# Kernel optimization log

Hardware: AMD Instinct MI355X
Metric: run time of the kernel (lower is better)

## Reference

```python
import jax, jax.numpy as jnp
import numpy as np

MAX_LEN = 3

def _attention(h, enc, w1, b1, w2):
    # h: [B,H], enc: [B,S,H]
    B, S, H = enc.shape
    hs = jnp.broadcast_to(h[:, None, :], (B, S, H))
    x = jnp.tanh(jnp.concatenate([enc, hs], axis=-1) @ w1.T + b1)  # [B,S,H]
    e = (x @ w2.T)[..., 0]                                         # [B,S]
    alpha = jax.nn.softmax(e, axis=1)
    return jnp.einsum('bs,bsd->bd', alpha, enc)                    # [B,H]

def _gru_cell(x, h, w_ih, w_hh, b_ih, b_hh):
    # torch GRU gate order: r, z, n
    H = h.shape[-1]
    gi = x @ w_ih.T + b_ih   # [B,3H]
    gh = h @ w_hh.T + b_hh
    i_r, i_z, i_n = gi[:, :H], gi[:, H:2*H], gi[:, 2*H:]
    h_r, h_z, h_n = gh[:, :H], gh[:, H:2*H], gh[:, 2*H:]
    r = jax.nn.sigmoid(i_r + h_r)
    z = jax.nn.sigmoid(i_z + h_z)
    n = jnp.tanh(i_n + r * h_n)
    return (1.0 - z) * n + z * h

def setup_inputs() -> dict:
    key = jax.random.key(0)
    ks = jax.random.split(key, 16)
    B, S, H, DW = 1024, 40, 1024, 512
    V0 = V1 = 4000
    EMB_N = V0 + V1 + 1
    sc = lambda fan: 1.0 / np.sqrt(fan)
    inp = {
        'encoder_outputs': jax.random.normal(ks[0], (B, S, H), jnp.float32),
        'encoder_hidden': jax.random.normal(ks[1], (1, B, H), jnp.float32),
        'targets': jax.random.randint(ks[2], (MAX_LEN, B), 0, V0),
        'emb': jax.random.normal(ks[3], (EMB_N, DW), jnp.float32) * 0.02,
        'attn_w1': jax.random.normal(ks[4], (H, 2 * H), jnp.float32) * sc(2 * H),
        'attn_b1': jnp.zeros((H,), jnp.float32),
        'attn_w2': jax.random.normal(ks[5], (1, H), jnp.float32) * sc(H),
        'w_ih': jax.random.normal(ks[6], (3 * H, H + DW), jnp.float32) * sc(H),
        'w_hh': jax.random.normal(ks[7], (3 * H, H), jnp.float32) * sc(H),
        'b_ih': jnp.zeros((3 * H,), jnp.float32),
        'b_hh': jnp.zeros((3 * H,), jnp.float32),
        'out0_w': jax.random.normal(ks[8], (V0, H), jnp.float32) * sc(H),
        'out0_b': jnp.zeros((V0,), jnp.float32),
        'out1_w': jax.random.normal(ks[9], (V1, H), jnp.float32) * sc(H),
        'out1_b': jnp.zeros((V1,), jnp.float32),
    }
    return inp

def reference(encoder_outputs, encoder_hidden, targets, emb, attn_w1, attn_b1,
              attn_w2, w_ih, w_hh, b_ih, b_hh, out0_w, out0_b, out1_w, out1_b):
    B = encoder_outputs.shape[0]
    h = encoder_hidden[0]  # n_layers=1, unidirectional -> init state passthrough
    logs = []
    for t in range(MAX_LEN):
        context = _attention(h, encoder_outputs, attn_w1, attn_b1, attn_w2)
        if t == 0:
            it = jnp.zeros((B,), jnp.int32)
        elif t == 1:
            it = targets[0] + 1
        else:
            it = targets[t - 1] + 36
        x = jnp.concatenate([emb[it], context], axis=1)  # [B, DW+H]
        h = _gru_cell(x, h, w_ih, w_hh, b_ih, b_hh)
        if t == 0 or t == 2:
            logits = h @ out0_w.T + out0_b
        else:
            logits = h @ out1_w.T + out1_b
        logs.append(jax.nn.log_softmax(logits, axis=1))
    return jnp.stack(logs)  # [MAX_LEN, B, V]
```

## Files before the change

kernel.cpp:

```cpp
#include <hip/hip_runtime.h>
#include <hip/hip_bf16.h>
#include <math.h>

#define B_SZ 1024
#define S_SZ 40
#define H_SZ 1024
#define DW_SZ 512
#define V_SZ 4000
#define XW (DW_SZ + H_SZ)
#define NGL 8192

typedef __bf16 bf16x8 __attribute__((ext_vector_type(8)));
typedef float f32x4 __attribute__((ext_vector_type(4)));

__device__ __forceinline__ float fast_tanh(float x) {
    return 1.0f - 2.0f / (1.0f + __expf(2.0f * x));
}
__device__ __forceinline__ float fast_sigmoid(float x) {
    return 1.0f / (1.0f + __expf(-x));
}
__device__ __forceinline__ float bfraw2f(unsigned short u) {
    return __uint_as_float(((unsigned)u) << 16);
}
__device__ __forceinline__ ushort4 cvt4(float4 v) {
    union { ushort4 u; __hip_bfloat16 h[4]; } o;
    o.h[0] = __float2bfloat16(v.x); o.h[1] = __float2bfloat16(v.y);
    o.h[2] = __float2bfloat16(v.z); o.h[3] = __float2bfloat16(v.w);
    return o.u;
}

#define GLL16(gp, lp)                                                                \
    __builtin_amdgcn_global_load_lds((const __attribute__((address_space(1))) void*)(gp), \
                                     (__attribute__((address_space(3))) void*)(lp), 16, 0, 0)

__global__ __launch_bounds__(256, 2) void gemm_bt_pipe128(
    const __hip_bfloat16* __restrict__ A, int lda,
    const __hip_bfloat16* __restrict__ W, int ldw,
    const float* __restrict__ bias,
    __hip_bfloat16* __restrict__ C, int ldc,
    int nbx, int K) {
    extern __shared__ char smem[];
    const int tid = threadIdx.x;
    const int lane = tid & 63;
    const int wave = tid >> 6;
    const int wm = wave >> 1, wn = wave & 1;
    const int fr = lane & 15, fq = lane >> 4;

    int bid = blockIdx.x;
    { const int cpx = gridDim.x >> 3; bid = (bid & 7) * cpx + (bid >> 3); }
    const int by = bid / nbx;
    const int bm = by * 128;
    const int bn = (bid - by * nbx) * 256;

    const int r0 = tid >> 2;
    const int s0 = (tid & 3) ^ ((tid >> 3) & 3);
    const __hip_bfloat16* gA0 = A + (size_t)(bm + r0) * lda + s0 * 8;
    const __hip_bfloat16* gA1 = A + (size_t)(bm + r0 + 64) * lda + s0 * 8;
    const __hip_bfloat16* gW0 = W + (size_t)(bn + r0) * ldw + s0 * 8;
    const __hip_bfloat16* gW1 = W + (size_t)(bn + r0 + 64) * ldw + s0 * 8;
    const __hip_bfloat16* gW2 = W + (size_t)(bn + r0 + 128) * ldw + s0 * 8;
    const __hip_bfloat16* gW3 = W + (size_t)(bn + r0 + 192) * ldw + s0 * 8;
    const int dst0 = tid * 16;

    int aoff[4], boff[8];
#pragma unroll
    for (int mi = 0; mi < 4; ++mi) {
        const int row = wm * 64 + mi * 16 + fr;
        aoff[mi] = row * 64 + ((fq ^ ((row >> 1) & 3)) << 4);
    }
#pragma unroll
    for (int ni = 0; ni < 8; ++ni) {
        const int col = wn * 128 + ni * 16 + fr;
        boff[ni] = 8192 + col * 64 + ((fq ^ ((col >> 1) & 3)) << 4);
    }

    const int NT = K >> 5;
    f32x4 acc[4][8] = {};

#define STAGE_T(t)                                                    \
    do {                                                              \
        char* sb = smem + ((t) % 3) * 24576;                          \
        const int kk = (t) << 5;                                      \
        GLL16(gA0 + kk, sb + dst0);                                   \
        GLL16(gA1 + kk, sb + dst0 + 4096);                            \
        GLL16(gW0 + kk, sb + 8192 + dst0);                            \
        GLL16(gW1 + kk, sb + 8192 + dst0 + 4096);                     \
        GLL16(gW2 + kk, sb + 8192 + dst0 + 8192);                     \
        GLL16(gW3 + kk, sb + 8192 + dst0 + 12288);                    \
    } while (0)

    STAGE_T(0);
    STAGE_T(1);
    __builtin_amdgcn_sched_barrier(0);
    asm volatile("s_waitcnt vmcnt(6)" ::: "memory");
    __builtin_amdgcn_s_barrier();
    __builtin_amdgcn_sched_barrier(0);

    for (int t = 0; t < NT; ++t) {
        const char* sb = smem + (t % 3) * 24576;
        bf16x8 af[4], bg[8];
#pragma unroll
        for (int ni = 0; ni < 8; ++ni) bg[ni] = *reinterpret_cast<const bf16x8*>(sb + boff[ni]);
#pragma unroll
        for (int mi = 0; mi < 4; ++mi) af[mi] = *reinterpret_cast<const bf16x8*>(sb + aoff[mi]);

        if (t + 2 < NT) STAGE_T(t + 2);

        __builtin_amdgcn_s_setprio(1);
#pragma unroll
        for (int mi = 0; mi < 4; ++mi)
#pragma unroll
            for (int ni = 0; ni < 8; ++ni)
                acc[mi][ni] = __builtin_amdgcn_mfma_f32_16x16x32_bf16(af[mi], bg[ni], acc[mi][ni], 0, 0, 0);
        __builtin_amdgcn_s_setprio(0);

        if (t != NT - 1) {
            __builtin_amdgcn_sched_barrier(0);
            if (t + 2 < NT) asm volatile("s_waitcnt vmcnt(6)" ::: "memory");
            else            asm volatile("s_waitcnt vmcnt(0)" ::: "memory");
            __builtin_amdgcn_s_barrier();
            __builtin_amdgcn_sched_barrier(0);
        }
    }
#undef STAGE_T

#pragma unroll
    for (int ni = 0; ni < 8; ++ni) {
        const int col = bn + wn * 128 + ni * 16 + fr;
        const float bb = bias ? bias[col] : 0.0f;
#pragma unroll
        for (int mi = 0; mi < 4; ++mi) {
            const int row0 = bm + wm * 64 + mi * 16 + fq * 4;
#pragma unroll
            for (int r = 0; r < 4; ++r)
                C[(size_t)(row0 + r) * ldc + col] = __float2bfloat16(acc[mi][ni][r] + bb);
        }
    }
}

#define SB0 0
#define SB1 10240
#define SB2 10496
#define SB3 10752
#define SB4 11520
#define SB5 12672
#define SB6 13672
#define SB7 14672
#define SB8 14696
#define SBTOT 14720
__global__ __launch_bounds__(256) void cast_fast_kernel(
    const float* __restrict__ enc, const float* __restrict__ w1,
    const float* __restrict__ whh, const float* __restrict__ wih,
    const float* __restrict__ o0, const float* __restrict__ o1,
    __hip_bfloat16* __restrict__ enc_bf, __hip_bfloat16* __restrict__ w1a_bf,
    __hip_bfloat16* __restrict__ wall0, __hip_bfloat16* __restrict__ wall1,
    __hip_bfloat16* __restrict__ wih_bf) {
    const int blk = blockIdx.x;
    const int tid = threadIdx.x;
    ushort4* w0u = reinterpret_cast<ushort4*>(wall0);
    ushort4* w1u = reinterpret_cast<ushort4*>(wall1);

    if (blk < SB1) {
        const int li = blk * 1024 + tid;
        const float4* s = reinterpret_cast<const float4*>(enc);
        float4 v0 = s[li], v1 = s[li + 256], v2 = s[li + 512], v3 = s[li + 768];
        ushort4* d = reinterpret_cast<ushort4*>(enc_bf);
        d[li] = cvt4(v0); d[li + 256] = cvt4(v1); d[li + 512] = cvt4(v2); d[li + 768] = cvt4(v3);
    } else if (blk < SB2) {
        const int r0 = (blk - SB1) * 4;
        const float4* s = reinterpret_cast<const float4*>(w1);
        float4 v0 = s[(r0 + 0) * 512 + tid], v1 = s[(r0 + 1) * 512 + tid],
               v2 = s[(r0 + 2) * 512 + tid], v3 = s[(r0 + 3) * 512 + tid];
        ushort4* d = reinterpret_cast<ushort4*>(w1a_bf);
        const int li = r0 * 256 + tid;
        d[li] = cvt4(v0); d[li + 256] = cvt4(v1); d[li + 512] = cvt4(v2); d[li + 768] = cvt4(v3);
    } else if (blk < SB3) {
        const int r0 = (blk - SB2) * 4;
        const float4* s = reinterpret_cast<const float4*>(w1);
        ushort4 u0 = cvt4(s[(r0 + 0) * 512 + 256 + tid]), u1 = cvt4(s[(r0 + 1) * 512 + 256 + tid]),
                u2 = cvt4(s[(r0 + 2) * 512 + 256 + tid]), u3 = cvt4(s[(r0 + 3) * 512 + 256 + tid]);
        const int li = r0 * 256 + tid;
        w0u[li] = u0; w0u[li + 256] = u1; w0u[li + 512] = u2; w0u[li + 768] = u3;
        w1u[li] = u0; w1u[li + 256] = u1; w1u[li + 512] = u2; w1u[li + 768] = u3;
    } else if (blk < SB4) {
        const int li = (blk - SB3) * 1024 + tid;
        const float4* s = reinterpret_cast<const float4*>(whh);
        ushort4 u0 = cvt4(s[li]), u1 = cvt4(s[li + 256]), u2 = cvt4(s[li + 512]), u3 = cvt4(s[li + 768]);
        w0u[262144 + li] = u0; w0u[262144 + li + 256] = u1;
        w0u[262144 + li + 512] = u2; w0u[262144 + li + 768] = u3;
        w1u[262144 + li] = u0; w1u[262144 + li + 256] = u1;
        w1u[262144 + li + 512] = u2; w1u[262144 + li + 768] = u3;
    } else if (blk < SB5) {
        const int li = (blk - SB4) * 1024 + tid;
        const float4* s = reinterpret_cast<const float4*>(wih);
        float4 v0 = s[li], v1 = s[li + 256], v2 = s[li + 512], v3 = s[li + 768];
        ushort4* d = reinterpret_cast<ushort4*>(wih_bf);
        d[li] = cvt4(v0); d[li + 256] = cvt4(v1); d[li + 512] = cvt4(v2); d[li + 768] = cvt4(v3);
    } else if (blk < SB6) {
        const int li = (blk - SB5) * 1024 + tid;
        const float4* s = reinterpret_cast<const float4*>(o0);
        float4 v0 = s[li], v1 = s[li + 256], v2 = s[li + 512], v3 = s[li + 768];
        w0u[1048576 + li] = cvt4(v0); w0u[1048576 + li + 256] = cvt4(v1);
        w0u[1048576 + li + 512] = cvt4(v2); w0u[1048576 + li + 768] = cvt4(v3);
    } else if (blk < SB7) {
        const int li = (blk - SB6) * 1024 + tid;
        const float4* s = reinterpret_cast<const float4*>(o1);
        float4 v0 = s[li], v1 = s[li + 256], v2 = s[li + 512], v3 = s[li + 768];
        w1u[1048576 + li] = cvt4(v0); w1u[1048576 + li + 256] = cvt4(v1);
        w1u[1048576 + li + 512] = cvt4(v2); w1u[1048576 + li + 768] = cvt4(v3);
    } else {
        const ushort4 z = make_ushort4(0, 0, 0, 0);
        if (blk < SB8) {
            const int li = 2072576 + (blk - SB7) * 1024 + tid;
            w0u[li] = z; w0u[li + 256] = z; w0u[li + 512] = z; w0u[li + 768] = z;
        } else {
            const int li = 2072576 + (blk - SB8) * 1024 + tid;
            w1u[li] = z; w1u[li + 256] = z; w1u[li + 512] = z; w1u[li + 768] = z;
        }
    }
}

__global__ __launch_bounds__(256) void small_prep_kernel(
    const float* __restrict__ emb, const int* __restrict__ targets,
    __hip_bfloat16* __restrict__ x0, __hip_bfloat16* __restrict__ x1, __hip_bfloat16* __restrict__ x2,
    const float* __restrict__ enc_h, float* __restrict__ h, __hip_bfloat16* __restrict__ h_bf,
    const float* __restrict__ b1, const float* __restrict__ b_hh,
    const float* __restrict__ o0b, const float* __restrict__ o1b,
    float* __restrict__ bias0, float* __restrict__ bias1) {
    const int blk = blockIdx.x;
    const int tid = threadIdx.x;
    if (blk < 3072) {
        if (tid >= 128) return;
        const int t = blk >> 10;
        const int b = blk & 1023;
        int it; __hip_bfloat16* x;
        if (t == 0) { it = 0; x = x0; }
        else if (t == 1) { it = targets[b] + 1; x = x1; }
        else { it = targets[B_SZ + b] + 36; x = x2; }
        float4 v = reinterpret_cast<const float4*>(emb + (size_t)it * DW_SZ)[tid];
        reinterpret_cast<ushort4*>(x + (size_t)b * XW)[tid] = cvt4(v);
    } else if (blk < 4096) {
        const int i = (blk - 3072) * 256 + tid;
        const float4 v = reinterpret_cast<const float4*>(enc_h)[i];
        reinterpret_cast<float4*>(h)[i] = v;
        reinterpret_cast<ushort4*>(h_bf)[i] = cvt4(v);
    } else {
        float* bt = (blk == 4096) ? bias0 : bias1;
        const float* ob = (blk == 4096) ? o0b : o1b;
        for (int j = tid; j < NGL; j += 256) {
            float v;
            if (j < H_SZ) v = b1[j];
            else if (j < 4 * H_SZ) v = b_hh[j - H_SZ];
            else if (j < 4 * H_SZ + V_SZ) v = ob[j - 4 * H_SZ];
            else v = 0.0f;
            bt[j] = v;
        }
    }
}

__global__ __launch_bounds__(256) void attn_ls_kernel(
    const __hip_bfloat16* __restrict__ enc,
    const __hip_bfloat16* __restrict__ enc_proj,
    const __hip_bfloat16* __restrict__ hgl,
    const float* __restrict__ w2,
    __hip_bfloat16* __restrict__ x,
    float* __restrict__ outp,
    int nattn) {
    const int blk = blockIdx.x;
    const int tid = threadIdx.x;
    const int lane = tid & 63, wave = tid >> 6;
    __shared__ float s_e[S_SZ];
    __shared__ float s_red[4];
    __shared__ float s_bc;

    if (blk < nattn) {
        const int b = blk;
        float hp[16], wv[16];
        const unsigned short* hgrow = reinterpret_cast<const unsigned short*>(hgl) + (size_t)b * NGL;
#pragma unroll
        for (int p = 0; p < 4; ++p) {
            const int base = p * 256 + lane * 4;
            ushort4 hu = *reinterpret_cast<const ushort4*>(hgrow + base);
            float4 wq = *reinterpret_cast<const float4*>(w2 + base);
            hp[p * 4 + 0] = bfraw2f(hu.x); hp[p * 4 + 1] = bfraw2f(hu.y);
            hp[p * 4 + 2] = bfraw2f(hu.z); hp[p * 4 + 3] = bfraw2f(hu.w);
            wv[p * 4 + 0] = wq.x; wv[p * 4 + 1] = wq.y;
            wv[p * 4 + 2] = wq.z; wv[p * 4 + 3] = wq.w;
        }

        const unsigned short* ep0 = reinterpret_cast<const unsigned short*>(enc_proj) + (size_t)b * S_SZ * H_SZ;
#pragma unroll 2
        for (int i = 0; i < 10; ++i) {
            const int s = wave + 4 * i;
            const unsigned short* row = ep0 + (size_t)s * H_SZ;
            float acc = 0.f;
#pragma unroll
            for (int p = 0; p < 4; ++p) {
                ushort4 eu = *reinterpret_cast<const ushort4*>(row + p * 256 + lane * 4);
                acc += fast_tanh(bfraw2f(eu.x) + hp[p * 4 + 0]) * wv[p * 4 + 0]
                     + fast_tanh(bfraw2f(eu.y) + hp[p * 4 + 1]) * wv[p * 4 + 1]
                     + fast_tanh(bfraw2f(eu.z) + hp[p * 4 + 2]) * wv[p * 4 + 2]
                     + fast_tanh(bfraw2f(eu.w) + hp[p * 4 + 3]) * wv[p * 4 + 3];
            }
#pragma unroll
            for (int off = 32; off > 0; off >>= 1) acc += __shfl_down(acc, off);
            if (lane == 0) s_e[s] = acc;
        }
        __syncthreads();

        float m = -1e30f;
        for (int s = 0; s < S_SZ; ++s) m = fmaxf(m, s_e[s]);
        float sum = 0.f;
        for (int s = 0; s < S_SZ; ++s) sum += __expf(s_e[s] - m);
        const float inv = 1.0f / sum;

        const ushort4* enc_b = reinterpret_cast<const ushort4*>(enc + (size_t)b * S_SZ * H_SZ);
        float4 acc = make_float4(0.f, 0.f, 0.f, 0.f);
        for (int s = 0; s < S_SZ; ++s) {
            const float a = __expf(s_e[s] - m) * inv;
            ushort4 ev = enc_b[s * 256 + tid];
            acc.x += a * bfraw2f(ev.x); acc.y += a * bfraw2f(ev.y);
            acc.z += a * bfraw2f(ev.z); acc.w += a * bfraw2f(ev.w);
        }
        reinterpret_cast<ushort4*>(x + (size_t)b * XW + DW_SZ)[tid] = cvt4(acc);
    } else {
        const int b = blk - nattn;
        const ushort4* row4 = reinterpret_cast<const ushort4*>(
            reinterpret_cast<const unsigned short*>(hgl) + (size_t)b * NGL + 4096);
        float* orow = outp + (size_t)b * V_SZ;

        float m = -1e30f;
        for (int k = tid; k < V_SZ / 4; k += 256) {
            ushort4 u = row4[k];
            m = fmaxf(m, fmaxf(fmaxf(bfraw2f(u.x), bfraw2f(u.y)), fmaxf(bfraw2f(u.z), bfraw2f(u.w))));
        }
#pragma unroll
        for (int off = 32; off > 0; off >>= 1) m = fmaxf(m, __shfl_down(m, off));
        if (lane == 0) s_red[wave] = m;
        __syncthreads();
        if (tid == 0) s_bc = fmaxf(fmaxf(s_red[0], s_red[1]), fmaxf(s_red[2], s_red[3]));
        __syncthreads();
        m = s_bc;

        float sum = 0.f;
        for (int k = tid; k < V_SZ / 4; k += 256) {
            ushort4 u = row4[k];
            sum += expf(bfraw2f(u.x) - m) + expf(bfraw2f(u.y) - m)
                 + expf(bfraw2f(u.z) - m) + expf(bfraw2f(u.w) - m);
        }
#pragma unroll
        for (int off = 32; off > 0; off >>= 1) sum += __shfl_down(sum, off);
        __syncthreads();
        if (lane == 0) s_red[wave] = sum;
        __syncthreads();
        if (tid == 0) s_bc = logf(s_red[0] + s_red[1] + s_red[2] + s_red[3]) + m;
        __syncthreads();
        const float ls = s_bc;

        for (int k = tid; k < V_SZ / 4; k += 256) {
            ushort4 u = row4[k];
            float4 o = make_float4(bfraw2f(u.x) - ls, bfraw2f(u.y) - ls,
                                   bfraw2f(u.z) - ls, bfraw2f(u.w) - ls);
            reinterpret_cast<float4*>(orow)[k] = o;
        }
    }
}

__global__ __launch_bounds__(256) void gru_gate_kernel(
    const __hip_bfloat16* __restrict__ gi,
    const __hip_bfloat16* __restrict__ hgl,
    float* __restrict__ h,
    __hip_bfloat16* __restrict__ h_bf) {
    const int idx = blockIdx.x * 256 + threadIdx.x;
    const int b = idx >> 10;
    const int j = idx & 1023;
    const unsigned short* gib = reinterpret_cast<const unsigned short*>(gi) + (size_t)b * 3 * H_SZ;
    const unsigned short* ghb = reinterpret_cast<const unsigned short*>(hgl) + (size_t)b * NGL + H_SZ;
    const float i_r = bfraw2f(gib[j]), i_z = bfraw2f(gib[H_SZ + j]), i_n = bfraw2f(gib[2 * H_SZ + j]);
    const float h_r = bfraw2f(ghb[j]), h_z = bfraw2f(ghb[H_SZ + j]), h_n = bfraw2f(ghb[2 * H_SZ + j]);
    const float r = fast_sigmoid(i_r + h_r);
    const float z = fast_sigmoid(i_z + h_z);
    const float n = fast_tanh(i_n + r * h_n);
    const float hv = (1.0f - z) * n + z * h[idx];
    h[idx] = hv;
    h_bf[idx] = __float2bfloat16(hv);
}

extern "C" void kernel_launch(void* const* d_in, const int* in_sizes, int n_in,
                              void* d_out, int out_size, void* d_ws, size_t ws_size,
                              hipStream_t stream) {
    const float* enc    = (const float*)d_in[0];
    const float* enc_h  = (const float*)d_in[1];
    const int*   tgt    = (const int*)d_in[2];
    const float* emb    = (const float*)d_in[3];
    const float* w1     = (const float*)d_in[4];
    const float* b1     = (const float*)d_in[5];
    const float* w2     = (const float*)d_in[6];
    const float* w_ih   = (const float*)d_in[7];
    const float* w_hh   = (const float*)d_in[8];
    const float* b_ih   = (const float*)d_in[9];
    const float* b_hh   = (const float*)d_in[10];
    const float* out0_w = (const float*)d_in[11];
    const float* out0_b = (const float*)d_in[12];
    const float* out1_w = (const float*)d_in[13];
    const float* out1_b = (const float*)d_in[14];
    float* out = (float*)d_out;

    char* wp = (char*)d_ws;
    auto carve = [&](size_t bytes) { char* p = wp; wp += (bytes + 255) & ~(size_t)255; return p; };
    __hip_bfloat16* enc_bf  = (__hip_bfloat16*)carve((size_t)B_SZ * S_SZ * H_SZ * 2);
    __hip_bfloat16* encp_bf = (__hip_bfloat16*)carve((size_t)B_SZ * S_SZ * H_SZ * 2);
    __hip_bfloat16* w1a_bf  = (__hip_bfloat16*)carve((size_t)H_SZ * H_SZ * 2);
    __hip_bfloat16* wall0   = (__hip_bfloat16*)carve((size_t)NGL * H_SZ * 2);
    __hip_bfloat16* wall1   = (__hip_bfloat16*)carve((size_t)NGL * H_SZ * 2);
    __hip_bfloat16* wih_bf  = (__hip_bfloat16*)carve((size_t)3 * H_SZ * XW * 2);
    float*          bias0   = (float*)carve((size_t)NGL * 4);
    float*          bias1   = (float*)carve((size_t)NGL * 4);
    float*          h       = (float*)carve((size_t)B_SZ * H_SZ * 4);
    __hip_bfloat16* h_bf    = (__hip_bfloat16*)carve((size_t)B_SZ * H_SZ * 2);
    __hip_bfloat16* hgl     = (__hip_bfloat16*)carve((size_t)B_SZ * NGL * 2);
    __hip_bfloat16* x_bf[3];
    for (int t = 0; t < 3; ++t) x_bf[t] = (__hip_bfloat16*)carve((size_t)B_SZ * XW * 2);
    __hip_bfloat16* gi_bf   = (__hip_bfloat16*)carve((size_t)B_SZ * 3 * H_SZ * 2);

    cast_fast_kernel<<<SBTOT, 256, 0, stream>>>(enc, w1, w_hh, w_ih, out0_w, out1_w,
                                                enc_bf, w1a_bf, wall0, wall1, wih_bf);
    small_prep_kernel<<<4098, 256, 0, stream>>>(emb, tgt, x_bf[0], x_bf[1], x_bf[2],
                                                enc_h, h, h_bf, b1, b_hh, out0_b, out1_b,
                                                bias0, bias1);

    gemm_bt_pipe128<<<(B_SZ * S_SZ / 128) * (H_SZ / 256), 256, 3 * 24576, stream>>>(
        enc_bf, H_SZ, w1a_bf, H_SZ, nullptr, encp_bf, H_SZ, H_SZ / 256, H_SZ);

    gemm_bt_pipe128<<<(B_SZ / 128) * 16, 256, 3 * 24576, stream>>>(
        h_bf, H_SZ, wall0, H_SZ, bias0, hgl, NGL, 16, H_SZ);

    attn_ls_kernel<<<B_SZ, 256, 0, stream>>>(enc_bf, encp_bf, hgl, w2, x_bf[0], out, B_SZ);

    for (int t = 0; t < 3; ++t) {
        gemm_bt_pipe128<<<(B_SZ / 128) * 12, 256, 3 * 24576, stream>>>(
            x_bf[t], XW, wih_bf, XW, b_ih, gi_bf, 3 * H_SZ, 12, XW);

        gru_gate_kernel<<<(B_SZ * H_SZ) / 256, 256, 0, stream>>>(gi_bf, hgl, h, h_bf);

        if (t == 0) {
            gemm_bt_pipe128<<<(B_SZ / 128) * 32, 256, 3 * 24576, stream>>>(
                h_bf, H_SZ, wall0, H_SZ, bias0, hgl, NGL, 32, H_SZ);
        } else if (t == 1) {
            gemm_bt_pipe128<<<(B_SZ / 128) * 32, 256, 3 * 24576, stream>>>(
                h_bf, H_SZ, wall1, H_SZ, bias1, hgl, NGL, 32, H_SZ);
        } else {
            gemm_bt_pipe128<<<(B_SZ / 128) * 16, 256, 3 * 24576, stream>>>(
                h_bf, H_SZ, wall0 + (size_t)4 * H_SZ * H_SZ, H_SZ, bias0 + 4 * H_SZ,
                hgl + 4 * H_SZ, NGL, 16, H_SZ);
        }

        float* outp = out + (size_t)t * B_SZ * V_SZ;
        if (t < 2) {
            attn_ls_kernel<<<2 * B_SZ, 256, 0, stream>>>(enc_bf, encp_bf, hgl, w2, x_bf[t + 1],
                                                         outp, B_SZ);
        } else {
            attn_ls_kernel<<<B_SZ, 256, 0, stream>>>(enc_bf, encp_bf, hgl, w2, x_bf[0],
                                                     outp, 0);
        }
    }
}
```

Measured before the change: 512.8 us.

## Add 512-thread GEMM variant for small-M GEMMs and merge prep kernels

Adds a second 128x256 bf16 MFMA GEMM kernel that runs 8 waves per block, each wave computing 64x64 of the tile instead of 64x128. It is used for the batch-size GEMMs (hidden-state and GRU input projections), whose grids are small and which stand to gain from more waves in flight and fewer accumulator registers per wave. The two setup kernels are also merged into one launch to cut a kernel dispatch. In exchange, each wave does less MFMA work per LDS fragment load, and with 512 threads and 72KB of LDS per block, occupancy may be limited.

```diff
diff --git a/kernel.cpp b/kernel.cpp
--- a/kernel.cpp
+++ b/kernel.cpp
@@ -33,7 +33,7 @@
     __builtin_amdgcn_global_load_lds((const __attribute__((address_space(1))) void*)(gp), \
                                      (__attribute__((address_space(3))) void*)(lp), 16, 0, 0)
 
-__global__ __launch_bounds__(256, 2) void gemm_bt_pipe128(
+__global__ __launch_bounds__(256, 2) void gemm_bt_pipe128_v1(
     const __hip_bfloat16* __restrict__ A, int lda,
     const __hip_bfloat16* __restrict__ W, int ldw,
     const float* __restrict__ bias,
@@ -138,6 +138,105 @@
     }
 }
 
+__global__ __launch_bounds__(512, 2) void gemm_bt_pipe128_v2(
+    const __hip_bfloat16* __restrict__ A, int lda,
+    const __hip_bfloat16* __restrict__ W, int ldw,
+    const float* __restrict__ bias,
+    __hip_bfloat16* __restrict__ C, int ldc,
+    int nbx, int K) {
+    extern __shared__ char smem[];
+    const int tid = threadIdx.x;
+    const int lane = tid & 63;
+    const int wave = tid >> 6;
+    const int wm = wave >> 2, wn = wave & 3;
+    const int fr = lane & 15, fq = lane >> 4;
+
+    int bid = blockIdx.x;
+    { const int cpx = gridDim.x >> 3; bid = (bid & 7) * cpx + (bid >> 3); }
+    const int by = bid / nbx;
+    const int bm = by * 128;
+    const int bn = (bid - by * nbx) * 256;
+
+    const int r0 = tid >> 2;
+    const int s0 = (tid & 3) ^ ((tid >> 3) & 3);
+    const __hip_bfloat16* gA0 = A + (size_t)(bm + r0) * lda + s0 * 8;
+    const __hip_bfloat16* gW0 = W + (size_t)(bn + r0) * ldw + s0 * 8;
+    const __hip_bfloat16* gW1 = W + (size_t)(bn + r0 + 128) * ldw + s0 * 8;
+    const int dst0 = tid * 16;
+
+    int aoff[4], boff[4];
+#pragma unroll
+    for (int mi = 0; mi < 4; ++mi) {
+        const int row = wm * 64 + mi * 16 + fr;
+        aoff[mi] = row * 64 + ((fq ^ ((row >> 1) & 3)) << 4);
+    }
+#pragma unroll
+    for (int ni = 0; ni < 4; ++ni) {
+        const int col = wn * 64 + ni * 16 + fr;
+        boff[ni] = 8192 + col * 64 + ((fq ^ ((col >> 1) & 3)) << 4);
+    }
+
+    const int NT = K >> 5;
+    f32x4 acc[4][4] = {};
+
+#define STAGE_T(t)                                                    \
+    do {                                                              \
+        char* sb = smem + ((t) % 3) * 24576;                          \
+        const int kk = (t) << 5;                                      \
+        GLL16(gA0 + kk, sb + dst0);                                   \
+        GLL16(gW0 + kk, sb + 8192 + dst0);                            \
+        GLL16(gW1 + kk, sb + 8192 + dst0 + 8192);                     \
+    } while (0)
+
+    STAGE_T(0);
+    STAGE_T(1);
+    __builtin_amdgcn_sched_barrier(0);
+    asm volatile("s_waitcnt vmcnt(3)" ::: "memory");
+    __builtin_amdgcn_s_barrier();
+    __builtin_amdgcn_sched_barrier(0);
+
+    for (int t = 0; t < NT; ++t) {
+        const char* sb = smem + (t % 3) * 24576;
+        bf16x8 af[4], bg[4];
+#pragma unroll
+        for (int ni = 0; ni < 4; ++ni) bg[ni] = *reinterpret_cast<const bf16x8*>(sb + boff[ni]);
+#pragma unroll
+        for (int mi = 0; mi < 4; ++mi) af[mi] = *reinterpret_cast<const bf16x8*>(sb + aoff[mi]);
+
+        if (t + 2 < NT) STAGE_T(t + 2);
+
+        __builtin_amdgcn_s_setprio(1);
+#pragma unroll
+        for (int mi = 0; mi < 4; ++mi)
+#pragma unroll
+            for (int ni = 0; ni < 4; ++ni)
+                acc[mi][ni] = __builtin_amdgcn_mfma_f32_16x16x32_bf16(af[mi], bg[ni], acc[mi][ni], 0, 0, 0);
+        __builtin_amdgcn_s_setprio(0);
+
+        if (t != NT - 1) {
+            __builtin_amdgcn_sched_barrier(0);
+            if (t + 2 < NT) asm volatile("s_waitcnt vmcnt(3)" ::: "memory");
+            else            asm volatile("s_waitcnt vmcnt(0)" ::: "memory");
+            __builtin_amdgcn_s_barrier();
+            __builtin_amdgcn_sched_barrier(0);
+        }
+    }
+#undef STAGE_T
+
+#pragma unroll
+    for (int ni = 0; ni < 4; ++ni) {
+        const int col = bn + wn * 64 + ni * 16 + fr;
+        const float bb = bias ? bias[col] : 0.0f;
+#pragma unroll
+        for (int mi = 0; mi < 4; ++mi) {
+            const int row0 = bm + wm * 64 + mi * 16 + fq * 4;
+#pragma unroll
+            for (int r = 0; r < 4; ++r)
+                C[(size_t)(row0 + r) * ldc + col] = __float2bfloat16(acc[mi][ni][r] + bb);
+        }
+    }
+}
+
 #define SB0 0
 #define SB1 10240
 #define SB2 10496
@@ -147,14 +246,23 @@
 #define SB6 13672
 #define SB7 14672
 #define SB8 14696
-#define SBTOT 14720
-__global__ __launch_bounds__(256) void cast_fast_kernel(
+#define SB9 14720
+#define SB10 (14720 + 3072)
+#define SB11 (SB10 + 1024)
+#define SBTOT (SB11 + 2)
+__global__ __launch_bounds__(256) void prep_kernel(
     const float* __restrict__ enc, const float* __restrict__ w1,
     const float* __restrict__ whh, const float* __restrict__ wih,
     const float* __restrict__ o0, const float* __restrict__ o1,
     __hip_bfloat16* __restrict__ enc_bf, __hip_bfloat16* __restrict__ w1a_bf,
     __hip_bfloat16* __restrict__ wall0, __hip_bfloat16* __restrict__ wall1,
-    __hip_bfloat16* __restrict__ wih_bf) {
+    __hip_bfloat16* __restrict__ wih_bf,
+    const float* __restrict__ emb, const int* __restrict__ targets,
+    __hip_bfloat16* __restrict__ x0, __hip_bfloat16* __restrict__ x1, __hip_bfloat16* __restrict__ x2,
+    const float* __restrict__ enc_h, float* __restrict__ h, __hip_bfloat16* __restrict__ h_bf,
+    const float* __restrict__ b1, const float* __restrict__ b_hh,
+    const float* __restrict__ o0b, const float* __restrict__ o1b,
+    float* __restrict__ bias0, float* __restrict__ bias1) {
     const int blk = blockIdx.x;
     const int tid = threadIdx.x;
     ushort4* w0u = reinterpret_cast<ushort4*>(wall0);
@@ -208,7 +316,7 @@
         float4 v0 = s[li], v1 = s[li + 256], v2 = s[li + 512], v3 = s[li + 768];
         w1u[1048576 + li] = cvt4(v0); w1u[1048576 + li + 256] = cvt4(v1);
         w1u[1048576 + li + 512] = cvt4(v2); w1u[1048576 + li + 768] = cvt4(v3);
-    } else {
+    } else if (blk < SB9) {
         const ushort4 z = make_ushort4(0, 0, 0, 0);
         if (blk < SB8) {
             const int li = 2072576 + (blk - SB7) * 1024 + tid;
@@ -217,36 +325,25 @@
             const int li = 2072576 + (blk - SB8) * 1024 + tid;
             w1u[li] = z; w1u[li + 256] = z; w1u[li + 512] = z; w1u[li + 768] = z;
         }
-    }
-}
-
-__global__ __launch_bounds__(256) void small_prep_kernel(
-    const float* __restrict__ emb, const int* __restrict__ targets,
-    __hip_bfloat16* __restrict__ x0, __hip_bfloat16* __restrict__ x1, __hip_bfloat16* __restrict__ x2,
-    const float* __restrict__ enc_h, float* __restrict__ h, __hip_bfloat16* __restrict__ h_bf,
-    const float* __restrict__ b1, const float* __restrict__ b_hh,
-    const float* __restrict__ o0b, const float* __restrict__ o1b,
-    float* __restrict__ bias0, float* __restrict__ bias1) {
-    const int blk = blockIdx.x;
-    const int tid = threadIdx.x;
-    if (blk < 3072) {
+    } else if (blk < SB10) {
         if (tid >= 128) return;
-        const int t = blk >> 10;
-        const int b = blk & 1023;
+        const int e = blk - SB9;
+        const int t = e >> 10;
+        const int b = e & 1023;
         int it; __hip_bfloat16* x;
         if (t == 0) { it = 0; x = x0; }
         else if (t == 1) { it = targets[b] + 1; x = x1; }
         else { it = targets[B_SZ + b] + 36; x = x2; }
         float4 v = reinterpret_cast<const float4*>(emb + (size_t)it * DW_SZ)[tid];
         reinterpret_cast<ushort4*>(x + (size_t)b * XW)[tid] = cvt4(v);
-    } else if (blk < 4096) {
-        const int i = (blk - 3072) * 256 + tid;
+    } else if (blk < SB11) {
+        const int i = (blk - SB10) * 256 + tid;
         const float4 v = reinterpret_cast<const float4*>(enc_h)[i];
         reinterpret_cast<float4*>(h)[i] = v;
         reinterpret_cast<ushort4*>(h_bf)[i] = cvt4(v);
     } else {
-        float* bt = (blk == 4096) ? bias0 : bias1;
-        const float* ob = (blk == 4096) ? o0b : o1b;
+        float* bt = (blk == SB11) ? bias0 : bias1;
+        const float* ob = (blk == SB11) ? o0b : o1b;
         for (int j = tid; j < NGL; j += 256) {
             float v;
             if (j < H_SZ) v = b1[j];
@@ -423,34 +520,34 @@
     for (int t = 0; t < 3; ++t) x_bf[t] = (__hip_bfloat16*)carve((size_t)B_SZ * XW * 2);
     __hip_bfloat16* gi_bf   = (__hip_bfloat16*)carve((size_t)B_SZ * 3 * H_SZ * 2);
 
-    cast_fast_kernel<<<SBTOT, 256, 0, stream>>>(enc, w1, w_hh, w_ih, out0_w, out1_w,
-                                                enc_bf, w1a_bf, wall0, wall1, wih_bf);
-    small_prep_kernel<<<4098, 256, 0, stream>>>(emb, tgt, x_bf[0], x_bf[1], x_bf[2],
-                                                enc_h, h, h_bf, b1, b_hh, out0_b, out1_b,
-                                                bias0, bias1);
-
-    gemm_bt_pipe128<<<(B_SZ * S_SZ / 128) * (H_SZ / 256), 256, 3 * 24576, stream>>>(
+    prep_kernel<<<SBTOT, 256, 0, stream>>>(enc, w1, w_hh, w_ih, out0_w, out1_w,
+                                           enc_bf, w1a_bf, wall0, wall1, wih_bf,
+                                           emb, tgt, x_bf[0], x_bf[1], x_bf[2],
+                                           enc_h, h, h_bf, b1, b_hh, out0_b, out1_b,
+                                           bias0, bias1);
+
+    gemm_bt_pipe128_v1<<<(B_SZ * S_SZ / 128) * (H_SZ / 256), 256, 3 * 24576, stream>>>(
         enc_bf, H_SZ, w1a_bf, H_SZ, nullptr, encp_bf, H_SZ, H_SZ / 256, H_SZ);
 
-    gemm_bt_pipe128<<<(B_SZ / 128) * 16, 256, 3 * 24576, stream>>>(
+    gemm_bt_pipe128_v2<<<(B_SZ / 128) * 16, 512, 3 * 24576, stream>>>(
         h_bf, H_SZ, wall0, H_SZ, bias0, hgl, NGL, 16, H_SZ);
 
     attn_ls_kernel<<<B_SZ, 256, 0, stream>>>(enc_bf, encp_bf, hgl, w2, x_bf[0], out, B_SZ);
 
     for (int t = 0; t < 3; ++t) {
-        gemm_bt_pipe128<<<(B_SZ / 128) * 12, 256, 3 * 24576, stream>>>(
+        gemm_bt_pipe128_v2<<<(B_SZ / 128) * 12, 512, 3 * 24576, stream>>>(
             x_bf[t], XW, wih_bf, XW, b_ih, gi_bf, 3 * H_SZ, 12, XW);
 
         gru_gate_kernel<<<(B_SZ * H_SZ) / 256, 256, 0, stream>>>(gi_bf, hgl, h, h_bf);
 
         if (t == 0) {
-            gemm_bt_pipe128<<<(B_SZ / 128) * 32, 256, 3 * 24576, stream>>>(
+            gemm_bt_pipe128_v2<<<(B_SZ / 128) * 32, 512, 3 * 24576, stream>>>(
                 h_bf, H_SZ, wall0, H_SZ, bias0, hgl, NGL, 32, H_SZ);
         } else if (t == 1) {
-            gemm_bt_pipe128<<<(B_SZ / 128) * 32, 256, 3 * 24576, stream>>>(
+            gemm_bt_pipe128_v2<<<(B_SZ / 128) * 32, 512, 3 * 24576, stream>>>(
                 h_bf, H_SZ, wall1, H_SZ, bias1, hgl, NGL, 32, H_SZ);
         } else {
-            gemm_bt_pipe128<<<(B_SZ / 128) * 16, 256, 3 * 24576, stream>>>(
+            gemm_bt_pipe128_v2<<<(B_SZ / 128) * 16, 512, 3 * 24576, stream>>>(
                 h_bf, H_SZ, wall0 + (size_t)4 * H_SZ * H_SZ, H_SZ, bias0 + 4 * H_SZ,
                 hgl + 4 * H_SZ, NGL, 16, H_SZ);
         }
```

Measured after the change: 490.0 us. 1.05x faster.
